# Optimization experiments

Hardware: AMD Instinct MI355X
Metric: run time of the kernel (lower is better)

The kernel has to match this reference:

```python
import jax, jax.numpy as jnp
import numpy as np

SCALES = (16, 32, 64, 128)
P = 8
D = 1024
H = 16
DEPTH = 8
MLP = 4096
NCLS = 1000
PB = [(s // P) ** 2 for s in SCALES]            # [4, 16, 64, 256]
BLOCKS = [PB[0] + 1] + PB[1:]                    # [5, 16, 64, 256]
L = sum(BLOCKS)                                  # 341
PATCH_L = sum(PB)                                # 340
PD = P * P * 3                                   # 192
HD = D // H
EPS = 1e-6

# scale id per token (start token belongs to scale 0)
_SID = np.concatenate([np.full(n, k, dtype=np.int32) for k, n in enumerate(BLOCKS)])
# additive block-causal mask: token in scale q may attend to scales <= q
_ALLOW = _SID[None, :] <= _SID[:, None]
MASK = jnp.where(jnp.asarray(_ALLOW), 0.0, -1e30).astype(jnp.float32)  # [L, L]
SID = jnp.asarray(_SID)


def _ln(x):
    m = jnp.mean(x, axis=-1, keepdims=True)
    v = jnp.var(x, axis=-1, keepdims=True)
    return (x - m) / jnp.sqrt(v + EPS)


def _l2n(t):
    n = jnp.sqrt(jnp.sum(t * t, axis=-1, keepdims=True))
    return t / jnp.maximum(n, 1e-12)


def setup_inputs() -> dict:
    key = jax.random.key(0)
    ks = jax.random.split(key, 16)
    s = 0.02
    inp = {
        "patches": jax.random.normal(ks[0], (8, PATCH_L, PD), jnp.float32),
        "labels": jax.random.randint(ks[1], (8,), 0, NCLS),
        "W_patch": s * jax.random.normal(ks[2], (PD, D), jnp.float32),
        "b_patch": jnp.zeros((D,), jnp.float32),
        "pos": s * jax.random.normal(ks[3], (1, L, D), jnp.float32),
        "scale_emb": s * jax.random.normal(ks[4], (len(SCALES), D), jnp.float32),
        "class_emb": s * jax.random.normal(ks[5], (NCLS + 1, D), jnp.float32),
        "ada_W": s * jax.random.normal(ks[6], (DEPTH, D, 6 * D), jnp.float32),
        "ada_b": jnp.zeros((DEPTH, 6 * D), jnp.float32),
        "qkv_W": s * jax.random.normal(ks[7], (DEPTH, D, 3 * D), jnp.float32),
        "qkv_b": jnp.zeros((DEPTH, 3 * D), jnp.float32),
        "q_scale": jnp.zeros((DEPTH, 1, 1, H, 1), jnp.float32),  # log-scale per head
        "proj_W": s * jax.random.normal(ks[8], (DEPTH, D, D), jnp.float32),
        "proj_b": jnp.zeros((DEPTH, D), jnp.float32),
        "fc1_W": s * jax.random.normal(ks[9], (DEPTH, D, MLP), jnp.float32),
        "fc1_b": jnp.zeros((DEPTH, MLP), jnp.float32),
        "fc2_W": s * jax.random.normal(ks[10], (DEPTH, MLP, D), jnp.float32),
        "fc2_b": jnp.zeros((DEPTH, D), jnp.float32),
        "head_ada_W": s * jax.random.normal(ks[11], (D, 2 * D), jnp.float32),
        "head_ada_b": jnp.zeros((2 * D,), jnp.float32),
        "head_W": s * jax.random.normal(ks[12], (D, PD), jnp.float32),
        "head_b": jnp.zeros((PD,), jnp.float32),
    }
    return inp


def reference(patches, labels, W_patch, b_patch, pos, scale_emb, class_emb,
              ada_W, ada_b, qkv_W, qkv_b, q_scale, proj_W, proj_b,
              fc1_W, fc1_b, fc2_W, fc2_b, head_ada_W, head_ada_b, head_W, head_b):
    B = patches.shape[0]
    cond = class_emb[labels]                              # [B, D]
    tok = patches @ W_patch + b_patch                     # [B, PATCH_L, D]
    x = jnp.concatenate([cond[:, None, :], tok], axis=1)  # [B, L, D]
    x = x + pos + scale_emb[SID]

    for i in range(DEPTH):
        ada = jax.nn.silu(cond) @ ada_W[i] + ada_b[i]     # [B, 6D]
        g1, g2, s1, s2, sh1, sh2 = [a[:, None, :] for a in jnp.split(ada, 6, axis=-1)]
        # attention branch
        h = _ln(x) * (s1 + 1.0) + sh1
        qkv = (h @ qkv_W[i] + qkv_b[i]).reshape(B, L, 3, H, HD)
        q, k, v = qkv[:, :, 0], qkv[:, :, 1], qkv[:, :, 2]  # [B, L, H, HD]
        q = _l2n(q) * jnp.exp(q_scale[i])                  # attn_l2_norm
        k = _l2n(k)
        scores = jnp.einsum("bqhd,bkhd->bhqk", q, k) + MASK
        attn = jax.nn.softmax(scores, axis=-1)
        o = jnp.einsum("bhqk,bkhd->bqhd", attn, v).reshape(B, L, D)
        x = x + g1 * (o @ proj_W[i] + proj_b[i])
        # mlp branch
        h2 = _ln(x) * (s2 + 1.0) + sh2
        m = jax.nn.gelu(h2 @ fc1_W[i] + fc1_b[i]) @ fc2_W[i] + fc2_b[i]
        x = x + g2 * m

    ada = jax.nn.silu(cond) @ head_ada_W + head_ada_b     # [B, 2D]
    sc, sh = [a[:, None, :] for a in jnp.split(ada, 2, axis=-1)]
    x = _ln(x) * (sc + 1.0) + sh
    return x @ head_W + head_b                            # [B, L, PD]
```

## Files before the change

kernel.cpp:

```cpp
#include <hip/hip_runtime.h>

typedef unsigned short ushort_t;
typedef __bf16 bf16x8 __attribute__((ext_vector_type(8)));
typedef float f32x4 __attribute__((ext_vector_type(4)));

#define DEV __device__ __forceinline__

DEV ushort_t f2bf(float x) {
  union { float f; unsigned u; } v; v.f = x;
  unsigned r = v.u + 0x7FFFu + ((v.u >> 16) & 1u);
  return (ushort_t)(r >> 16);
}
DEV int sid_of(int l) { return l < 5 ? 0 : (l < 21 ? 1 : (l < 85 ? 2 : 3)); }
DEV float fast_tanh(float u) { return 1.0f - 2.0f / (__expf(2.0f * u) + 1.0f); }
DEV float gelu_f(float x) {
  float u = 0.7978845608028654f * (x + 0.044715f * x * x * x);
  return 0.5f * x * (1.0f + fast_tanh(u));
}
DEV float silu_f(float x) { return x / (1.0f + __expf(-x)); }
DEV f32x4 mfma16(bf16x8 a, bf16x8 b, f32x4 c) {
  return __builtin_amdgcn_mfma_f32_16x16x32_bf16(a, b, c, 0, 0, 0);
}
DEV void gload16(const void* src, void* dst) {
  __builtin_amdgcn_global_load_lds(
      (const __attribute__((address_space(1))) void*)(uintptr_t)src,
      (__attribute__((address_space(3))) void*)(uintptr_t)dst, 16, 0, 0);
}

__global__ __launch_bounds__(256) void k_cond_x0(
    const int* __restrict__ labels, const float* __restrict__ class_emb,
    const float* __restrict__ pos, const float* __restrict__ semb,
    float* __restrict__ cond, float* __restrict__ x) {
  int b = blockIdx.x, t = threadIdx.x;
  int lab = labels[b];
  float4 cv = *(const float4*)&class_emb[(size_t)lab * 1024 + t * 4];
  *(float4*)&cond[(size_t)b * 1024 + t * 4] = cv;
  float4 pv = *(const float4*)&pos[t * 4];
  float4 sv = *(const float4*)&semb[t * 4];
  float4 xv;
  xv.x = cv.x + pv.x + sv.x; xv.y = cv.y + pv.y + sv.y;
  xv.z = cv.z + pv.z + sv.z; xv.w = cv.w + pv.w + sv.w;
  *(float4*)&x[(size_t)b * 341 * 1024 + t * 4] = xv;
}

__global__ __launch_bounds__(256) void k_convert(const float* __restrict__ src,
                                                 ushort_t* __restrict__ dst, int n4) {
  int i = blockIdx.x * 256 + threadIdx.x;
  if (i < n4) {
    float4 v = *(const float4*)&src[(size_t)i * 4];
    uint2 pk;
    pk.x = (unsigned)f2bf(v.x) | ((unsigned)f2bf(v.y) << 16);
    pk.y = (unsigned)f2bf(v.z) | ((unsigned)f2bf(v.w) << 16);
    *(uint2*)&dst[(size_t)i * 4] = pk;
  }
}

__global__ __launch_bounds__(256) void k_transpose(const float* __restrict__ src,
                                                   ushort_t* __restrict__ dst, int K, int N) {
  __shared__ ushort_t tile[32][33];
  int z = blockIdx.z;
  src += (size_t)z * K * N;
  dst += (size_t)z * K * N;
  int k0 = blockIdx.y * 32, n0 = blockIdx.x * 32;
  int t = threadIdx.x;
  int r = t >> 3, c = (t & 7) * 4;
  float4 v = *(const float4*)&src[(size_t)(k0 + r) * N + n0 + c];
  tile[r][c] = f2bf(v.x); tile[r][c + 1] = f2bf(v.y);
  tile[r][c + 2] = f2bf(v.z); tile[r][c + 3] = f2bf(v.w);
  __syncthreads();
  ushort_t o0 = tile[c][r], o1 = tile[c + 1][r], o2 = tile[c + 2][r], o3 = tile[c + 3][r];
  uint2 pk;
  pk.x = (unsigned)o0 | ((unsigned)o1 << 16);
  pk.y = (unsigned)o2 | ((unsigned)o3 << 16);
  *(uint2*)&dst[(size_t)(n0 + r) * K + k0 + c] = pk;
}

__global__ __launch_bounds__(256) void k_ada(const float* __restrict__ cond,
    const float* __restrict__ ada_W, const float* __restrict__ ada_b,
    const float* __restrict__ hada_W, const float* __restrict__ hada_b,
    float* __restrict__ ada_out, float* __restrict__ hada_out) {
  int gy = blockIdx.y;
  bool head = (gy == 8);
  int Nw = head ? 2048 : 6144;
  int n0 = blockIdx.x * 64;
  if (n0 >= Nw) return;
  __shared__ float sc[8 * 1024];
  __shared__ float red[4][64][8];
  int t = threadIdx.x;
  for (int i = t; i < 2048; i += 256) {
    float4 cv = *(const float4*)&cond[(size_t)i * 4];
    float* d = &sc[i * 4];
    d[0] = silu_f(cv.x); d[1] = silu_f(cv.y); d[2] = silu_f(cv.z); d[3] = silu_f(cv.w);
  }
  __syncthreads();
  const float* W = head ? hada_W : ada_W + (size_t)gy * 1024 * 6144;
  const float* bs = head ? hada_b : ada_b + (size_t)gy * 6144;
  float* op = head ? hada_out : ada_out + (size_t)gy * 8 * 6144;
  int col = n0 + (t & 63), kq = t >> 6;
  float acc[8] = {0.f, 0.f, 0.f, 0.f, 0.f, 0.f, 0.f, 0.f};
  for (int k = kq * 256; k < kq * 256 + 256; ++k) {
    float wv = W[(size_t)k * Nw + col];
#pragma unroll
    for (int b2 = 0; b2 < 8; ++b2) acc[b2] += wv * sc[b2 * 1024 + k];
  }
#pragma unroll
  for (int b2 = 0; b2 < 8; ++b2) red[kq][t & 63][b2] = acc[b2];
  __syncthreads();
  if (t < 64) {
    int colc = n0 + t;
    float bias = bs[colc];
#pragma unroll
    for (int b2 = 0; b2 < 8; ++b2) {
      float v = red[0][t][b2] + red[1][t][b2] + red[2][t][b2] + red[3][t][b2] + bias;
      op[(size_t)b2 * Nw + colc] = v;
    }
  }
}

__global__ __launch_bounds__(256) void k_ln(const float* __restrict__ x,
    ushort_t* __restrict__ hout, const float* __restrict__ ada,
    int stride, int soff, int shoff) {
  int row = blockIdx.x, t = threadIdx.x;
  int b = row / 341;
  const float* xr = x + (size_t)row * 1024;
  float4 xv = *(const float4*)&xr[t * 4];
  float s = xv.x + xv.y + xv.z + xv.w;
  float ss = xv.x * xv.x + xv.y * xv.y + xv.z * xv.z + xv.w * xv.w;
#pragma unroll
  for (int off = 1; off < 64; off <<= 1) { s += __shfl_xor(s, off); ss += __shfl_xor(ss, off); }
  __shared__ float red[8];
  int w = t >> 6, lane = t & 63;
  if (lane == 0) { red[w] = s; red[w + 4] = ss; }
  __syncthreads();
  s = red[0] + red[1] + red[2] + red[3];
  ss = red[4] + red[5] + red[6] + red[7];
  float mean = s * (1.f / 1024.f);
  float var = ss * (1.f / 1024.f) - mean * mean;
  float rstd = rsqrtf(var + 1e-6f);
  const float* ar = ada + (size_t)b * stride;
  float xe[4] = {xv.x, xv.y, xv.z, xv.w};
  ushort_t tmp[4];
#pragma unroll
  for (int j = 0; j < 4; ++j) {
    int n = t * 4 + j;
    float val = (xe[j] - mean) * rstd * (1.f + ar[soff + n]) + ar[shoff + n];
    tmp[j] = f2bf(val);
  }
  uint2 pk;
  pk.x = (unsigned)tmp[0] | ((unsigned)tmp[1] << 16);
  pk.y = (unsigned)tmp[2] | ((unsigned)tmp[3] << 16);
  *(uint2*)&hout[(size_t)row * 1024 + t * 4] = pk;
}

__global__ __launch_bounds__(256) void k_comb_ln(
    const float* __restrict__ p, const float* __restrict__ bias,
    const float* __restrict__ adag, int goff,
    float* __restrict__ x, const float* __restrict__ adaln,
    int lnstride, int soff, int shoff,
    ushort_t* __restrict__ hout) {
  int row = blockIdx.x, t = threadIdx.x;
  int b = row / 341;
  int c = t * 4;
  float4 s4 = *(const float4*)&p[(size_t)row * 1024 + c];
  float4 q2 = *(const float4*)&p[(size_t)2728 * 1024 + (size_t)row * 1024 + c];
  s4.x += q2.x; s4.y += q2.y; s4.z += q2.z; s4.w += q2.w;
  float4 bv = *(const float4*)&bias[c];
  const float* gr = adag + (size_t)b * 6144 + goff + c;
  float4 xv = *(float4*)&x[(size_t)row * 1024 + c];
  xv.x += gr[0] * (s4.x + bv.x);
  xv.y += gr[1] * (s4.y + bv.y);
  xv.z += gr[2] * (s4.z + bv.z);
  xv.w += gr[3] * (s4.w + bv.w);
  *(float4*)&x[(size_t)row * 1024 + c] = xv;
  float sm = xv.x + xv.y + xv.z + xv.w;
  float ss = xv.x * xv.x + xv.y * xv.y + xv.z * xv.z + xv.w * xv.w;
#pragma unroll
  for (int off = 1; off < 64; off <<= 1) { sm += __shfl_xor(sm, off); ss += __shfl_xor(ss, off); }
  __shared__ float red[8];
  int w = t >> 6, lane = t & 63;
  if (lane == 0) { red[w] = sm; red[w + 4] = ss; }
  __syncthreads();
  sm = red[0] + red[1] + red[2] + red[3];
  ss = red[4] + red[5] + red[6] + red[7];
  float mean = sm * (1.f / 1024.f);
  float var = ss * (1.f / 1024.f) - mean * mean;
  float rstd = rsqrtf(var + 1e-6f);
  const float* ar = adaln + (size_t)b * lnstride;
  float xe[4] = {xv.x, xv.y, xv.z, xv.w};
  ushort_t tmp[4];
#pragma unroll
  for (int j = 0; j < 4; ++j) {
    int n = c + j;
    float val = (xe[j] - mean) * rstd * (1.f + ar[soff + n]) + ar[shoff + n];
    tmp[j] = f2bf(val);
  }
  uint2 pk;
  pk.x = (unsigned)tmp[0] | ((unsigned)tmp[1] << 16);
  pk.y = (unsigned)tmp[2] | ((unsigned)tmp[3] << 16);
  *(uint2*)&hout[(size_t)row * 1024 + c] = pk;
}

template <int EPI, int BM>
__global__ __launch_bounds__(256, 3) void k_gemm(
    const ushort_t* __restrict__ A, const ushort_t* __restrict__ Bt,
    const float* __restrict__ bias, float* __restrict__ fout,
    ushort_t* __restrict__ bfout, const float* __restrict__ aux,
    float* __restrict__ xres, const float* __restrict__ pos,
    const float* __restrict__ semb, int M, int N, int K, int KS) {
  constexpr int NI = (BM == 128) ? 4 : 2;
  constexpr int WNB = (BM == 128) ? 64 : 32;
  __shared__ ushort_t aT[2][BM * 32];
  __shared__ ushort_t bT[2][128 * 32];
  int tid = threadIdx.x;
  int lane = tid & 63, w = tid >> 6;
  int WR = (BM == 128) ? (w >> 1) : 0;
  int WC = (BM == 128) ? (w & 1) : w;

  int gx = gridDim.x;
  int nwg = gx * gridDim.y;
  int orig = blockIdx.y * gx + blockIdx.x;
  int q = nwg >> 3, r8 = nwg & 7;
  int xcd = orig & 7, idx = orig >> 3;
  int lin = (xcd < r8 ? xcd * (q + 1) : r8 * (q + 1) + (xcd - r8) * q) + idx;
  int bx = lin % gx, by = lin / gx;

  int m0 = by * BM, n0 = bx * 128;
  int kbase = blockIdx.z * KS;
  f32x4 acc[4][NI];
#pragma unroll
  for (int i = 0; i < 4; ++i)
#pragma unroll
    for (int j = 0; j < NI; ++j) acc[i][j] = (f32x4){0.f, 0.f, 0.f, 0.f};

  int lrow = lane & 15;
  int csw = (lrow >> 1) & 3;
  int coff = ((lane >> 4) ^ csw) * 8;

  int s_row0 = tid >> 2, s_u = tid & 3;
  int s_c = s_u ^ ((s_row0 >> 1) & 3);
  int aR0 = m0 + s_row0; if (aR0 > M - 1) aR0 = M - 1;
  int bR0 = n0 + s_row0; if (bR0 > N - 1) bR0 = N - 1;
  int aR1 = m0 + s_row0 + 64; if (aR1 > M - 1) aR1 = M - 1;
  int bR1 = n0 + s_row0 + 64; if (bR1 > N - 1) bR1 = N - 1;
  const ushort_t* aSrc0 = A + (size_t)aR0 * K + kbase + s_c * 8;
  const ushort_t* aSrc1 = A + (size_t)aR1 * K + kbase + s_c * 8;
  const ushort_t* bSrc0 = Bt + (size_t)bR0 * K + kbase + s_c * 8;
  const ushort_t* bSrc1 = Bt + (size_t)bR1 * K + kbase + s_c * 8;
  int slot0 = w * 512, slot1 = 2048 + w * 512;

  int nsteps = KS >> 5;
  auto STAGE = [&](int k0, int buf) {
    gload16(aSrc0 + k0, &aT[buf][slot0]);
    if constexpr (BM == 128) gload16(aSrc1 + k0, &aT[buf][slot1]);
    gload16(bSrc0 + k0, &bT[buf][slot0]);
    gload16(bSrc1 + k0, &bT[buf][slot1]);
  };

  STAGE(0, 0);
  int cur = 0;
  for (int s = 0; s < nsteps; ++s) {
    int kn = (s + 1 < nsteps) ? ((s + 1) << 5) : 0;
    STAGE(kn, cur ^ 1);
    if constexpr (BM == 128)
      asm volatile("s_waitcnt vmcnt(4)" ::: "memory");
    else
      asm volatile("s_waitcnt vmcnt(3)" ::: "memory");
    __builtin_amdgcn_sched_barrier(0);
    __builtin_amdgcn_s_barrier();
    __builtin_amdgcn_sched_barrier(0);
    bf16x8 af[4], bb[NI];
#pragma unroll
    for (int mi = 0; mi < 4; ++mi)
      af[mi] = *(const bf16x8*)&aT[cur][(WR * 64 + mi * 16 + lrow) * 32 + coff];
#pragma unroll
    for (int ni = 0; ni < NI; ++ni)
      bb[ni] = *(const bf16x8*)&bT[cur][(WC * WNB + ni * 16 + lrow) * 32 + coff];
#pragma unroll
    for (int mi = 0; mi < 4; ++mi)
#pragma unroll
      for (int ni = 0; ni < NI; ++ni)
        acc[mi][ni] = mfma16(af[mi], bb[ni], acc[mi][ni]);
    __builtin_amdgcn_sched_barrier(0);
    __builtin_amdgcn_s_barrier();
    __builtin_amdgcn_sched_barrier(0);
    cur ^= 1;
  }

  if constexpr (EPI == 6) {
    int nb = n0 + WC * 64;
    int gh = nb >> 6;
    float qse = (gh < 16) ? __expf(aux[gh]) : 1.0f;
    bool dn = gh < 32;
#pragma unroll
    for (int mi = 0; mi < 4; ++mi) {
#pragma unroll
      for (int r = 0; r < 4; ++r) {
        float vv[4]; float ss = 0.f;
#pragma unroll
        for (int ni = 0; ni < 4; ++ni) {
          vv[ni] = acc[mi][ni][r] + bias[nb + ni * 16 + lrow];
          ss += vv[ni] * vv[ni];
        }
        if (dn) {
          ss += __shfl_xor(ss, 1); ss += __shfl_xor(ss, 2);
          ss += __shfl_xor(ss, 4); ss += __shfl_xor(ss, 8);
          float rn = qse / fmaxf(sqrtf(ss), 1e-12f);
#pragma unroll
          for (int ni = 0; ni < 4; ++ni) vv[ni] *= rn;
        }
        int gm = m0 + WR * 64 + mi * 16 + (lane >> 4) * 4 + r;
        if (gm < M) {
#pragma unroll
          for (int ni = 0; ni < 4; ++ni)
            bfout[(size_t)gm * N + nb + ni * 16 + lrow] = f2bf(vv[ni]);
        }
      }
    }
  } else {
#pragma unroll
    for (int mi = 0; mi < 4; ++mi) {
#pragma unroll
      for (int ni = 0; ni < NI; ++ni) {
#pragma unroll
        for (int r = 0; r < 4; ++r) {
          int gm = m0 + WR * 64 + mi * 16 + (lane >> 4) * 4 + r;
          int gn = n0 + WC * WNB + ni * 16 + lrow;
          if (gm >= M || gn >= N) continue;
          if constexpr (EPI == 7) {
            fout[(size_t)blockIdx.z * M * N + (size_t)gm * N + gn] = acc[mi][ni][r];
          } else {
            float v = acc[mi][ni][r] + bias[gn];
            if constexpr (EPI == 1) {
              int b = gm / 341;
              xres[(size_t)gm * 1024 + gn] += aux[(size_t)b * 6144 + gn] * v;
            } else if constexpr (EPI == 2) {
              bfout[(size_t)gm * N + gn] = f2bf(gelu_f(v));
            } else if constexpr (EPI == 4) {
              int b = gm / 340, l = gm % 340 + 1;
              float val = v + pos[(size_t)l * 1024 + gn] + semb[(size_t)sid_of(l) * 1024 + gn];
              xres[((size_t)(b * 341 + l)) * 1024 + gn] = val;
            }
          }
        }
      }
    }
  }
}

__global__ __launch_bounds__(256) void k_comb_head(const float* __restrict__ p,
    const float* __restrict__ bias, float* __restrict__ out, int nsplit) {
  int row = blockIdx.x, t = threadIdx.x;
  const int N = 192;
  size_t stride = (size_t)2728 * N;
  if (t < 48) {
    int c = t * 4;
    float4 s = *(const float4*)&p[(size_t)row * N + c];
    for (int sp = 1; sp < nsplit; ++sp) {
      float4 qq = *(const float4*)&p[sp * stride + (size_t)row * N + c];
      s.x += qq.x; s.y += qq.y; s.z += qq.z; s.w += qq.w;
    }
    float4 bv = *(const float4*)&bias[c];
    s.x += bv.x; s.y += bv.y; s.z += bv.z; s.w += bv.w;
    *(float4*)&out[(size_t)row * N + c] = s;
  }
}

__global__ __launch_bounds__(256) void k_attn(
    const ushort_t* __restrict__ qkv, ushort_t* __restrict__ o) {
  int qt = blockIdx.x, h = blockIdx.y, b = blockIdx.z;
  int t = threadIdx.x, lane = t & 63, w = t >> 6;
  int q0 = qt * 64;
  __shared__ ushort_t qT[64 * 72], kT[64 * 72], vS[64 * 72], vT[64 * 72];
  __shared__ ushort_t pT[4][16 * 72];
#pragma unroll
  for (int i = 0; i < 2; ++i) {
    int vid = t + 256 * i;
    int row = vid >> 3, seg = (vid & 7) * 8;
    int l = q0 + row; if (l > 340) l = 340;
    uint4 v = *(const uint4*)&qkv[((size_t)(b * 341 + l)) * 3072 + h * 64 + seg];
    *(uint4*)&qT[row * 72 + seg] = v;
  }
  int lrow = lane & 15, lk8 = (lane >> 4) * 8;
  int sq[4];
  float mrun[4], lsum[4];
  f32x4 accO[4];
#pragma unroll
  for (int r = 0; r < 4; ++r) {
    int lq = q0 + w * 16 + (lane >> 4) * 4 + r;
    sq[r] = sid_of(lq < 341 ? lq : 340);
    mrun[r] = -1e30f;
    lsum[r] = 0.f;
  }
#pragma unroll
  for (int d = 0; d < 4; ++d) accO[d] = (f32x4){0.f, 0.f, 0.f, 0.f};
  int nch = (qt == 0) ? 2 : 6;
  int vd = t >> 2, vlseg = (t & 3) * 16;
  for (int c = 0; c < nch; ++c) {
    __syncthreads();
#pragma unroll
    for (int i = 0; i < 2; ++i) {
      int vid = t + 256 * i;
      int row = vid >> 3, seg = (vid & 7) * 8;
      int l = c * 64 + row; if (l > 340) l = 340;
      size_t base = ((size_t)(b * 341 + l)) * 3072 + h * 64 + seg;
      uint4 kv = *(const uint4*)&qkv[base + 1024];
      uint4 vv = *(const uint4*)&qkv[base + 2048];
      *(uint4*)&kT[row * 72 + seg] = kv;
      *(uint4*)&vS[row * 72 + seg] = vv;
    }
    __syncthreads();
    ushort_t tmp[16];
#pragma unroll
    for (int j = 0; j < 16; ++j) tmp[j] = vS[(vlseg + j) * 72 + vd];
    f32x4 sf[4];
#pragma unroll
    for (int nf = 0; nf < 4; ++nf) sf[nf] = (f32x4){0.f, 0.f, 0.f, 0.f};
    __builtin_amdgcn_s_setprio(1);
#pragma unroll
    for (int ks = 0; ks < 2; ++ks) {
      bf16x8 aq = *(const bf16x8*)&qT[(w * 16 + lrow) * 72 + ks * 32 + lk8];
#pragma unroll
      for (int nf = 0; nf < 4; ++nf) {
        bf16x8 bk = *(const bf16x8*)&kT[(nf * 16 + lrow) * 72 + ks * 32 + lk8];
        sf[nf] = mfma16(aq, bk, sf[nf]);
      }
    }
    __builtin_amdgcn_s_setprio(0);
#pragma unroll
    for (int nf = 0; nf < 4; ++nf) {
      int lk = c * 64 + nf * 16 + lrow;
      int sk = lk < 341 ? sid_of(lk) : 9;
#pragma unroll
      for (int r = 0; r < 4; ++r)
        if (sk > sq[r]) sf[nf][r] = -1e30f;
    }
    float rs[4];
#pragma unroll
    for (int r = 0; r < 4; ++r) {
      float m = sf[0][r];
      m = fmaxf(m, sf[1][r]); m = fmaxf(m, sf[2][r]); m = fmaxf(m, sf[3][r]);
#pragma unroll
      for (int off = 1; off < 16; off <<= 1) m = fmaxf(m, __shfl_xor(m, off));
      float mn = fmaxf(mrun[r], m);
      float scl = __expf(mrun[r] - mn);
      mrun[r] = mn;
      lsum[r] *= scl;
#pragma unroll
      for (int d = 0; d < 4; ++d) accO[d][r] *= scl;
      rs[r] = 0.f;
    }
    ushort_t* pw = &pT[w][0];
#pragma unroll
    for (int nf = 0; nf < 4; ++nf) {
#pragma unroll
      for (int r = 0; r < 4; ++r) {
        float p = __expf(sf[nf][r] - mrun[r]);
        rs[r] += p;
        pw[((lane >> 4) * 4 + r) * 72 + nf * 16 + lrow] = f2bf(p);
      }
    }
#pragma unroll
    for (int r = 0; r < 4; ++r) {
      float sum = rs[r];
#pragma unroll
      for (int off = 1; off < 16; off <<= 1) sum += __shfl_xor(sum, off);
      lsum[r] += sum;
    }
    {
      uint4 s0, s1;
      s0.x = (unsigned)tmp[0] | ((unsigned)tmp[1] << 16);
      s0.y = (unsigned)tmp[2] | ((unsigned)tmp[3] << 16);
      s0.z = (unsigned)tmp[4] | ((unsigned)tmp[5] << 16);
      s0.w = (unsigned)tmp[6] | ((unsigned)tmp[7] << 16);
      s1.x = (unsigned)tmp[8] | ((unsigned)tmp[9] << 16);
      s1.y = (unsigned)tmp[10] | ((unsigned)tmp[11] << 16);
      s1.z = (unsigned)tmp[12] | ((unsigned)tmp[13] << 16);
      s1.w = (unsigned)tmp[14] | ((unsigned)tmp[15] << 16);
      *(uint4*)&vT[vd * 72 + vlseg] = s0;
      *(uint4*)&vT[vd * 72 + vlseg + 8] = s1;
    }
    __syncthreads();
    __builtin_amdgcn_s_setprio(1);
#pragma unroll
    for (int ks = 0; ks < 2; ++ks) {
      bf16x8 ap = *(const bf16x8*)&pw[lrow * 72 + ks * 32 + lk8];
#pragma unroll
      for (int d = 0; d < 4; ++d) {
        bf16x8 bv = *(const bf16x8*)&vT[(d * 16 + lrow) * 72 + ks * 32 + lk8];
        accO[d] = mfma16(ap, bv, accO[d]);
      }
    }
    __builtin_amdgcn_s_setprio(0);
  }
#pragma unroll
  for (int d = 0; d < 4; ++d) {
#pragma unroll
    for (int r = 0; r < 4; ++r) {
      int lq = q0 + w * 16 + (lane >> 4) * 4 + r;
      if (lq < 341) {
        float ov = accO[d][r] / fmaxf(lsum[r], 1e-30f);
        o[((size_t)(b * 341 + lq)) * 1024 + h * 64 + d * 16 + lrow] = f2bf(ov);
      }
    }
  }
}

extern "C" void kernel_launch(void* const* d_in, const int* in_sizes, int n_in,
                              void* d_out, int out_size, void* d_ws, size_t ws_size,
                              hipStream_t stream) {
  const float* patches   = (const float*)d_in[0];
  const int*   labels    = (const int*)d_in[1];
  const float* W_patch   = (const float*)d_in[2];
  const float* b_patch   = (const float*)d_in[3];
  const float* pos       = (const float*)d_in[4];
  const float* scale_emb = (const float*)d_in[5];
  const float* class_emb = (const float*)d_in[6];
  const float* ada_W     = (const float*)d_in[7];
  const float* ada_b     = (const float*)d_in[8];
  const float* qkv_W     = (const float*)d_in[9];
  const float* qkv_b     = (const float*)d_in[10];
  const float* q_scale   = (const float*)d_in[11];
  const float* proj_W    = (const float*)d_in[12];
  const float* proj_b    = (const float*)d_in[13];
  const float* fc1_W     = (const float*)d_in[14];
  const float* fc1_b     = (const float*)d_in[15];
  const float* fc2_W     = (const float*)d_in[16];
  const float* fc2_b     = (const float*)d_in[17];
  const float* hada_W    = (const float*)d_in[18];
  const float* hada_b    = (const float*)d_in[19];
  const float* head_W    = (const float*)d_in[20];
  const float* head_b    = (const float*)d_in[21];
  (void)in_sizes; (void)n_in; (void)out_size; (void)ws_size;

  char* wsb = (char*)d_ws;
  size_t off = 0;
  auto alloc = [&](size_t bytes) -> void* {
    void* p = wsb + off;
    off = (off + bytes + 255) & ~(size_t)255;
    return p;
  };

  float*    f_cond   = (float*)alloc(8 * 1024 * 4);
  float*    f_ada    = (float*)alloc((size_t)8 * 8 * 6144 * 4);
  float*    f_hada   = (float*)alloc(8 * 2048 * 4);
  float*    f_x      = (float*)alloc((size_t)2728 * 1024 * 4);
  ushort_t* u_h      = (ushort_t*)alloc((size_t)2728 * 1024 * 2);
  ushort_t* u_qkv    = (ushort_t*)alloc((size_t)2728 * 3072 * 2);
  ushort_t* u_o      = (ushort_t*)alloc((size_t)2728 * 1024 * 2);
  ushort_t* u_mid    = (ushort_t*)alloc((size_t)2728 * 4096 * 2);
  float*    f_part   = (float*)alloc((size_t)2 * 2728 * 1024 * 4);
  ushort_t* u_patch  = (ushort_t*)alloc((size_t)2720 * 192 * 2);
  ushort_t* u_qkvt   = (ushort_t*)alloc((size_t)8 * 3072 * 1024 * 2);
  ushort_t* u_projt  = (ushort_t*)alloc((size_t)8 * 1024 * 1024 * 2);
  ushort_t* u_fc1t   = (ushort_t*)alloc((size_t)8 * 4096 * 1024 * 2);
  ushort_t* u_fc2t   = (ushort_t*)alloc((size_t)8 * 1024 * 4096 * 2);
  ushort_t* u_wpt    = (ushort_t*)alloc((size_t)1024 * 192 * 2);
  ushort_t* u_wht    = (ushort_t*)alloc((size_t)192 * 1024 * 2);

  const int MT = 22;
  const int MT64 = 43;

  k_cond_x0<<<8, 256, 0, stream>>>(labels, class_emb, pos, scale_emb, f_cond, f_x);
  k_transpose<<<dim3(32, 6, 1), 256, 0, stream>>>(W_patch, u_wpt, 192, 1024);
  k_transpose<<<dim3(6, 32, 1), 256, 0, stream>>>(head_W, u_wht, 1024, 192);
  k_convert<<<510, 256, 0, stream>>>(patches, u_patch, 130560);
  k_ada<<<dim3(96, 9), 256, 0, stream>>>(f_cond, ada_W, ada_b, hada_W, hada_b, f_ada, f_hada);
  k_transpose<<<dim3(96, 32, 8), 256, 0, stream>>>(qkv_W, u_qkvt, 1024, 3072);
  k_transpose<<<dim3(32, 32, 8), 256, 0, stream>>>(proj_W, u_projt, 1024, 1024);
  k_transpose<<<dim3(128, 32, 8), 256, 0, stream>>>(fc1_W, u_fc1t, 1024, 4096);
  k_transpose<<<dim3(32, 128, 8), 256, 0, stream>>>(fc2_W, u_fc2t, 4096, 1024);

  k_gemm<4, 128><<<dim3(8, MT), 256, 0, stream>>>(u_patch, u_wpt, b_patch, nullptr, nullptr,
                                                  nullptr, f_x, pos, scale_emb, 2720, 1024, 192, 192);
  k_ln<<<2728, 256, 0, stream>>>(f_x, u_h, f_ada, 6144, 2048, 4096);

  for (int i = 0; i < 8; ++i) {
    const float* adaL = f_ada + (size_t)i * 8 * 6144;
    k_gemm<6, 128><<<dim3(24, MT), 256, 0, stream>>>(u_h, u_qkvt + (size_t)i * 3072 * 1024,
                                                     qkv_b + (size_t)i * 3072, nullptr, u_qkv,
                                                     q_scale + (size_t)i * 16, nullptr, nullptr,
                                                     nullptr, 2728, 3072, 1024, 1024);
    k_attn<<<dim3(6, 16, 8), 256, 0, stream>>>(u_qkv, u_o);
    k_gemm<1, 64><<<dim3(8, MT64, 1), 256, 0, stream>>>(u_o, u_projt + (size_t)i * 1024 * 1024,
                                                        proj_b + (size_t)i * 1024, nullptr,
                                                        nullptr, adaL, f_x, nullptr, nullptr,
                                                        2728, 1024, 1024, 1024);
    k_ln<<<2728, 256, 0, stream>>>(f_x, u_h, adaL, 6144, 3072, 5120);
    k_gemm<2, 128><<<dim3(32, MT), 256, 0, stream>>>(u_h, u_fc1t + (size_t)i * 4096 * 1024,
                                                     fc1_b + (size_t)i * 4096, nullptr,
                                                     u_mid, nullptr, nullptr, nullptr, nullptr,
                                                     2728, 4096, 1024, 1024);
    k_gemm<7, 64><<<dim3(8, MT64, 2), 256, 0, stream>>>(u_mid, u_fc2t + (size_t)i * 4096 * 1024,
                                                        nullptr, f_part, nullptr, nullptr,
                                                        nullptr, nullptr, nullptr,
                                                        2728, 1024, 4096, 2048);
    if (i < 7) {
      k_comb_ln<<<2728, 256, 0, stream>>>(f_part, fc2_b + (size_t)i * 1024, adaL, 1024,
                                          f_x, f_ada + (size_t)(i + 1) * 8 * 6144,
                                          6144, 2048, 4096, u_h);
    } else {
      k_comb_ln<<<2728, 256, 0, stream>>>(f_part, fc2_b + (size_t)i * 1024, adaL, 1024,
                                          f_x, f_hada, 2048, 0, 1024, u_h);
    }
  }

  k_gemm<7, 64><<<dim3(2, MT64, 4), 256, 0, stream>>>(u_h, u_wht, nullptr, f_part, nullptr,
                                                      nullptr, nullptr, nullptr, nullptr,
                                                      2728, 192, 1024, 256);
  k_comb_head<<<2728, 256, 0, stream>>>(f_part, head_b, (float*)d_out, 4);
}
```

Measured before the change: 1.780 ms.

## Add 512-thread 128x256-tile GEMM with XCD-aware block remap for QKV/FC1/FC2

Adds a new GEMM kernel with 8 waves per block and 128x256 output tiles, which doubles the N-tile width so each A tile loaded into shared memory is reused across more columns. It also remaps block indices so consecutive tiles are grouped per XCD, aiming for better L2 locality. The QKV, FC1 and FC2 GEMMs switch to this kernel, while the proj and head GEMMs keep the old kernel. Larger tiles mean fewer blocks in the grid and more shared memory and register pressure per block, which can reduce occupancy or wave-quantization efficiency.

Measured after the change: 1.876 ms. 5.3% more time.

```diff
diff --git a/kernel.cpp b/kernel.cpp
--- a/kernel.cpp
+++ b/kernel.cpp
@@ -286,10 +286,115 @@
     cur ^= 1;
   }
 
+#pragma unroll
+  for (int mi = 0; mi < 4; ++mi) {
+#pragma unroll
+    for (int ni = 0; ni < NI; ++ni) {
+#pragma unroll
+      for (int r = 0; r < 4; ++r) {
+        int gm = m0 + WR * 64 + mi * 16 + (lane >> 4) * 4 + r;
+        int gn = n0 + WC * WNB + ni * 16 + lrow;
+        if (gm >= M || gn >= N) continue;
+        if constexpr (EPI == 7) {
+          fout[(size_t)blockIdx.z * M * N + (size_t)gm * N + gn] = acc[mi][ni][r];
+        } else {
+          float v = acc[mi][ni][r] + bias[gn];
+          if constexpr (EPI == 1) {
+            int b = gm / 341;
+            xres[(size_t)gm * 1024 + gn] += aux[(size_t)b * 6144 + gn] * v;
+          } else if constexpr (EPI == 2) {
+            bfout[(size_t)gm * N + gn] = f2bf(gelu_f(v));
+          } else if constexpr (EPI == 4) {
+            int b = gm / 340, l = gm % 340 + 1;
+            float val = v + pos[(size_t)l * 1024 + gn] + semb[(size_t)sid_of(l) * 1024 + gn];
+            xres[((size_t)(b * 341 + l)) * 1024 + gn] = val;
+          }
+        }
+      }
+    }
+  }
+}
+
+template <int EPI>
+__global__ __launch_bounds__(512, 4) void k_gemm2(
+    const ushort_t* __restrict__ A, const ushort_t* __restrict__ Bt,
+    const float* __restrict__ bias, float* __restrict__ fout,
+    ushort_t* __restrict__ bfout, const float* __restrict__ aux,
+    int M, int N, int K, int KS) {
+  __shared__ ushort_t aT[2][128 * 32];
+  __shared__ ushort_t bT[2][256 * 32];
+  int tid = threadIdx.x;
+  int lane = tid & 63, w = tid >> 6;
+  int WR = w >> 2, WC = w & 3;
+
+  int gx = gridDim.x;
+  int nwg = gx * gridDim.y;
+  int orig = blockIdx.y * gx + blockIdx.x;
+  int q = nwg >> 3, r8 = nwg & 7;
+  int xcd = orig & 7, idx = orig >> 3;
+  int lin = (xcd < r8 ? xcd * (q + 1) : r8 * (q + 1) + (xcd - r8) * q) + idx;
+  int bx = lin % gx, by = lin / gx;
+
+  int m0 = by * 128, n0 = bx * 256;
+  int kbase = blockIdx.z * KS;
+  f32x4 acc[4][4];
+#pragma unroll
+  for (int i = 0; i < 4; ++i)
+#pragma unroll
+    for (int j = 0; j < 4; ++j) acc[i][j] = (f32x4){0.f, 0.f, 0.f, 0.f};
+
+  int lrow = lane & 15;
+  int csw = (lrow >> 1) & 3;
+  int coff = ((lane >> 4) ^ csw) * 8;
+
+  int s_row0 = tid >> 2, s_u = tid & 3;
+  int s_c = s_u ^ ((s_row0 >> 1) & 3);
+  int aR0 = m0 + s_row0; if (aR0 > M - 1) aR0 = M - 1;
+  int bR0 = n0 + s_row0; if (bR0 > N - 1) bR0 = N - 1;
+  int bR1 = n0 + s_row0 + 128; if (bR1 > N - 1) bR1 = N - 1;
+  const ushort_t* aSrc0 = A + (size_t)aR0 * K + kbase + s_c * 8;
+  const ushort_t* bSrc0 = Bt + (size_t)bR0 * K + kbase + s_c * 8;
+  const ushort_t* bSrc1 = Bt + (size_t)bR1 * K + kbase + s_c * 8;
+  int slot = w * 512;
+
+  int nsteps = KS >> 5;
+  auto STAGE = [&](int k0, int buf) {
+    gload16(aSrc0 + k0, &aT[buf][slot]);
+    gload16(bSrc0 + k0, &bT[buf][slot]);
+    gload16(bSrc1 + k0, &bT[buf][4096 + slot]);
+  };
+
+  STAGE(0, 0);
+  int cur = 0;
+  for (int s = 0; s < nsteps; ++s) {
+    int kn = (s + 1 < nsteps) ? ((s + 1) << 5) : 0;
+    STAGE(kn, cur ^ 1);
+    asm volatile("s_waitcnt vmcnt(3)" ::: "memory");
+    __builtin_amdgcn_sched_barrier(0);
+    __builtin_amdgcn_s_barrier();
+    __builtin_amdgcn_sched_barrier(0);
+    bf16x8 af[4], bb[4];
+#pragma unroll
+    for (int mi = 0; mi < 4; ++mi)
+      af[mi] = *(const bf16x8*)&aT[cur][(WR * 64 + mi * 16 + lrow) * 32 + coff];
+#pragma unroll
+    for (int ni = 0; ni < 4; ++ni)
+      bb[ni] = *(const bf16x8*)&bT[cur][(WC * 64 + ni * 16 + lrow) * 32 + coff];
+#pragma unroll
+    for (int mi = 0; mi < 4; ++mi)
+#pragma unroll
+      for (int ni = 0; ni < 4; ++ni)
+        acc[mi][ni] = mfma16(af[mi], bb[ni], acc[mi][ni]);
+    __builtin_amdgcn_sched_barrier(0);
+    __builtin_amdgcn_s_barrier();
+    __builtin_amdgcn_sched_barrier(0);
+    cur ^= 1;
+  }
+
   if constexpr (EPI == 6) {
     int nb = n0 + WC * 64;
     int gh = nb >> 6;
-    float qse = (gh < 16) ? __expf(aux[gh]) : 1.0f;
+    float qse = (gh < 16) ? __expf(aux[gh & 15]) : 1.0f;
     bool dn = gh < 32;
 #pragma unroll
     for (int mi = 0; mi < 4; ++mi) {
@@ -320,26 +425,16 @@
 #pragma unroll
     for (int mi = 0; mi < 4; ++mi) {
 #pragma unroll
-      for (int ni = 0; ni < NI; ++ni) {
+      for (int ni = 0; ni < 4; ++ni) {
 #pragma unroll
         for (int r = 0; r < 4; ++r) {
           int gm = m0 + WR * 64 + mi * 16 + (lane >> 4) * 4 + r;
-          int gn = n0 + WC * WNB + ni * 16 + lrow;
+          int gn = n0 + WC * 64 + ni * 16 + lrow;
           if (gm >= M || gn >= N) continue;
           if constexpr (EPI == 7) {
             fout[(size_t)blockIdx.z * M * N + (size_t)gm * N + gn] = acc[mi][ni][r];
-          } else {
-            float v = acc[mi][ni][r] + bias[gn];
-            if constexpr (EPI == 1) {
-              int b = gm / 341;
-              xres[(size_t)gm * 1024 + gn] += aux[(size_t)b * 6144 + gn] * v;
-            } else if constexpr (EPI == 2) {
-              bfout[(size_t)gm * N + gn] = f2bf(gelu_f(v));
-            } else if constexpr (EPI == 4) {
-              int b = gm / 340, l = gm % 340 + 1;
-              float val = v + pos[(size_t)l * 1024 + gn] + semb[(size_t)sid_of(l) * 1024 + gn];
-              xres[((size_t)(b * 341 + l)) * 1024 + gn] = val;
-            }
+          } else if constexpr (EPI == 2) {
+            bfout[(size_t)gm * N + gn] = f2bf(gelu_f(acc[mi][ni][r] + bias[gn]));
           }
         }
       }
@@ -576,24 +671,21 @@
 
   for (int i = 0; i < 8; ++i) {
     const float* adaL = f_ada + (size_t)i * 8 * 6144;
-    k_gemm<6, 128><<<dim3(24, MT), 256, 0, stream>>>(u_h, u_qkvt + (size_t)i * 3072 * 1024,
-                                                     qkv_b + (size_t)i * 3072, nullptr, u_qkv,
-                                                     q_scale + (size_t)i * 16, nullptr, nullptr,
-                                                     nullptr, 2728, 3072, 1024, 1024);
+    k_gemm2<6><<<dim3(12, MT), 512, 0, stream>>>(u_h, u_qkvt + (size_t)i * 3072 * 1024,
+                                                 qkv_b + (size_t)i * 3072, nullptr, u_qkv,
+                                                 q_scale + (size_t)i * 16, 2728, 3072, 1024, 1024);
     k_attn<<<dim3(6, 16, 8), 256, 0, stream>>>(u_qkv, u_o);
     k_gemm<1, 64><<<dim3(8, MT64, 1), 256, 0, stream>>>(u_o, u_projt + (size_t)i * 1024 * 1024,
                                                         proj_b + (size_t)i * 1024, nullptr,
                                                         nullptr, adaL, f_x, nullptr, nullptr,
                                                         2728, 1024, 1024, 1024);
     k_ln<<<2728, 256, 0, stream>>>(f_x, u_h, adaL, 6144, 3072, 5120);
-    k_gemm<2, 128><<<dim3(32, MT), 256, 0, stream>>>(u_h, u_fc1t + (size_t)i * 4096 * 1024,
-                                                     fc1_b + (size_t)i * 4096, nullptr,
-                                                     u_mid, nullptr, nullptr, nullptr, nullptr,
-                                                     2728, 4096, 1024, 1024);
-    k_gemm<7, 64><<<dim3(8, MT64, 2), 256, 0, stream>>>(u_mid, u_fc2t + (size_t)i * 4096 * 1024,
-                                                        nullptr, f_part, nullptr, nullptr,
-                                                        nullptr, nullptr, nullptr,
-                                                        2728, 1024, 4096, 2048);
+    k_gemm2<2><<<dim3(16, MT), 512, 0, stream>>>(u_h, u_fc1t + (size_t)i * 4096 * 1024,
+                                                 fc1_b + (size_t)i * 4096, nullptr, u_mid,
+                                                 nullptr, 2728, 4096, 1024, 1024);
+    k_gemm2<7><<<dim3(4, MT, 2), 512, 0, stream>>>(u_mid, u_fc2t + (size_t)i * 4096 * 1024,
+                                                   nullptr, f_part, nullptr, nullptr,
+                                                   2728, 1024, 4096, 2048);
     if (i < 7) {
       k_comb_ln<<<2728, 256, 0, stream>>>(f_part, fc2_b + (size_t)i * 1024, adaL, 1024,
                                           f_x, f_ada + (size_t)(i + 1) * 8 * 6144,
```
